# Optimization experiments

Hardware: AMD Instinct MI355X
Metric: run time of the kernel (lower is better)

Reference implementation:

```python
import jax, jax.numpy as jnp
import numpy as np
import math

DIMS = 128
S = 2                     # scalar_attention_num
VS = 0.25                 # voxel_size
QS = 0.01                 # quant_size
L = int((2 * VS + 0.0001) // QS)   # 50, quant table length
GRID = int(2 / VS)        # 8
G = GRID ** 3             # 512 voxel groups
K = 32                    # points per voxel (regularized)
B = 2
N = G * K                 # 16384 points per cloud


def setup_inputs() -> dict:
    key = jax.random.key(0)
    ks = jax.random.split(key, 12)
    inputs = jax.random.normal(ks[0], (B, N, DIMS), jnp.float32)
    # coordinates scaled so per-voxel pairwise distances lie in (-VS, VS)
    coordinates = jax.random.uniform(ks[1], (B, N, 3), jnp.float32) * VS
    # groups: partition of the N points into G voxels of K points each
    groups = jnp.tile(jnp.arange(N, dtype=jnp.int32).reshape(1, G, K), (B, 1, 1))
    effective_groups = jnp.tile(jnp.arange(G, dtype=jnp.int32)[None], (B, 1))
    qkv_w = jax.random.normal(ks[2], (S, DIMS, 3 * DIMS), jnp.float32) * 0.02
    qkv_b = jnp.zeros((S, 3 * DIMS), jnp.float32)
    table_x = jax.random.normal(ks[3], (S, 3, L, DIMS), jnp.float32) * 0.02
    table_y = jax.random.normal(ks[4], (S, 3, L, DIMS), jnp.float32) * 0.02
    table_z = jax.random.normal(ks[5], (S, 3, L, DIMS), jnp.float32) * 0.02
    trans_w = jax.random.normal(ks[6], (DIMS * (S + 1), DIMS), jnp.float32) * 0.02
    trans_b = jnp.zeros((DIMS,), jnp.float32)
    ln_g = jnp.ones((DIMS,), jnp.float32)
    ln_b = jnp.zeros((DIMS,), jnp.float32)
    return {"inputs": inputs, "coordinates": coordinates, "qkv_w": qkv_w,
            "qkv_b": qkv_b, "table_x": table_x, "table_y": table_y,
            "table_z": table_z, "trans_w": trans_w, "trans_b": trans_b,
            "ln_g": ln_g, "ln_b": ln_b, "groups": groups,
            "effective_groups": effective_groups}


def reference(inputs, coordinates, qkv_w, qkv_b, table_x, table_y, table_z,
              trans_w, trans_b, ln_g, ln_b, groups, effective_groups):
    B_, N_, d = inputs.shape
    # gather points per voxel: [B,G,K,d] / [B,G,K,3]
    gflat = groups.reshape(B_, -1)
    feats = jnp.take_along_axis(inputs, gflat[..., None], axis=1).reshape(B_, G, K, d)
    coords = jnp.take_along_axis(coordinates, gflat[..., None], axis=1).reshape(B_, G, K, 3)
    # pairwise distances within each voxel: [B,G,K,K,3]
    dist = coords[:, :, :, None, :] - coords[:, :, None, :, :]
    idx = jnp.clip(jnp.floor((dist + VS) / QS).astype(jnp.int32), 0, L - 1)
    f = feats
    x = feats
    for s in range(S):
        qkv = f @ qkv_w[s] + qkv_b[s]                  # [B,G,K,3d]
        q, k, v = jnp.split(qkv, 3, axis=-1)
        enc = (table_x[s, 1][idx[..., 0]]
               + table_y[s, 1][idx[..., 1]]
               + table_z[s, 1][idx[..., 2]])           # [B,G,K,K,d]
        bias = jnp.einsum('bgid,bgijd->bgij', k, enc)
        scores = (jnp.einsum('bgid,bgjd->bgij', q, k) + bias) / math.sqrt(d)
        attn = jax.nn.softmax(scores, axis=-1)
        f = jnp.einsum('bgij,bgjd->bgid', attn, v)
        x = jnp.concatenate([x, f], axis=-1)
    # trans: Linear -> LayerNorm -> ReLU, then max-pool over points
    h = x @ trans_w + trans_b
    mu = jnp.mean(h, axis=-1, keepdims=True)
    var = jnp.var(h, axis=-1, keepdims=True)
    h = (h - mu) / jnp.sqrt(var + 1e-5) * ln_g + ln_b
    h = jax.nn.relu(h)
    pooled = jnp.max(h, axis=2)                        # [B,G,d]
    # group index i = m*GRID^2 + n*GRID + t ; output grid at [t,n,m]
    grid = pooled.reshape(B_, GRID, GRID, GRID, d).transpose(0, 3, 2, 1, 4)
    out = grid.reshape(B_, -1, d)                      # [B, GRID^3, d]
    # per-point retrieve buffer: scatter pooled feature back to each point
    for_ret = jnp.zeros((B_, N_, d), inputs.dtype)
    b_idx = jnp.arange(B_)[:, None, None]
    for_ret = for_ret.at[b_idx, groups].set(
        jnp.broadcast_to(pooled[:, :, None, :], (B_, G, K, d)))
    return out, for_ret
```

## Files before the change

kernel.cpp:

```cpp
#include <hip/hip_runtime.h>
#include <cstddef>


#define D_   128
#define VSF  0.25f
#define QSF  0.01f
#define LQ   50
#define G_   512
#define KP   32
#define BB   2
#define NP   16384
#define MT   32768
#define SCALE 0.08838834764831845f
#define NT_ALL 34
#define FRAG_S (NT_ALL * 4 * 64 * 8)

using short8 = __attribute__((ext_vector_type(8))) short;
using f32x4  = __attribute__((ext_vector_type(4))) float;

__device__ inline unsigned short f2bf(float x) {
  unsigned u = __builtin_bit_cast(unsigned, x);
  u += 0x7fffu + ((u >> 16) & 1u);
  return (unsigned short)(u >> 16);
}
__device__ inline float bu(unsigned short h) {
  return __builtin_bit_cast(float, (unsigned)h << 16);
}
__device__ inline short8 as_short8(uint4 v) {
  union { uint4 u; short8 s; } x; x.u = v; return x.s;
}

__global__ __launch_bounds__(256) void prep_tt(
    const float* __restrict__ tbl_x, const float* __restrict__ tbl_y,
    const float* __restrict__ tbl_z, float* __restrict__ Tt)
{
  const int c = threadIdx.x;
  const int s = blockIdx.x >> 7;
  const int e = blockIdx.x & 127;
  float v = 0.f;
  if (c < 150) {
    const int axis = c / 50, l = c - axis * 50;
    const float* tb = (axis == 0 ? tbl_x : (axis == 1 ? tbl_y : tbl_z));
    v = tb[(((size_t)s * 3 + 1) * LQ + l) * D_ + e];
  }
  Tt[((size_t)(s * 128 + e)) * 256 + c] = v;
}

__global__ __launch_bounds__(256) void wf_gemm(
    const float* __restrict__ qkv_w, const float* __restrict__ Tt,
    float* __restrict__ Wf)
{
  __shared__ __align__(16) float A_s[16][68];
  __shared__ __align__(16) float B_s[16][132];
  const int t  = threadIdx.x;
  const int s  = blockIdx.z;
  const float* A = qkv_w + (size_t)s * 128 * 384 + 128;
  const float* B = Tt + (size_t)s * 128 * 256;
  float* C       = Wf + (size_t)s * 128 * 256;
  const int m0 = blockIdx.x * 64;
  const int n0 = blockIdx.y * 128;
  const int r  = t >> 2;
  const int kq = (t & 3) * 4;
  const float* arow = A + (size_t)(m0 + r) * 384;
  const int kkb = t >> 4;
  const int cb  = (t & 15) * 8;
  const float* wbase = B + (size_t)kkb * 256 + n0 + cb;
  const int tx = t & 31, ty = t >> 5;

  float acc[8][4];
  #pragma unroll
  for (int i = 0; i < 8; i++)
    #pragma unroll
    for (int j = 0; j < 4; j++) acc[i][j] = 0.f;

  for (int k0 = 0; k0 < 128; k0 += 16) {
    float4 av = *(const float4*)(arow + k0 + kq);
    float4 b0 = *(const float4*)(wbase + (size_t)k0 * 256);
    float4 b1 = *(const float4*)(wbase + (size_t)k0 * 256 + 4);
    __syncthreads();
    A_s[kq + 0][r] = av.x;
    A_s[kq + 1][r] = av.y;
    A_s[kq + 2][r] = av.z;
    A_s[kq + 3][r] = av.w;
    *(float4*)&B_s[kkb][cb]     = b0;
    *(float4*)&B_s[kkb][cb + 4] = b1;
    __syncthreads();
    #pragma unroll
    for (int kk = 0; kk < 16; kk++) {
      float4 a03 = *(const float4*)&A_s[kk][ty * 8];
      float4 a47 = *(const float4*)&A_s[kk][ty * 8 + 4];
      float4 bv  = *(const float4*)&B_s[kk][tx * 4];
      float a[8] = {a03.x, a03.y, a03.z, a03.w, a47.x, a47.y, a47.z, a47.w};
      float bj[4] = {bv.x, bv.y, bv.z, bv.w};
      #pragma unroll
      for (int i = 0; i < 8; i++)
        #pragma unroll
        for (int j = 0; j < 4; j++)
          acc[i][j] += a[i] * bj[j];
    }
  }
  #pragma unroll
  for (int i = 0; i < 8; i++) {
    float4 o = {acc[i][0], acc[i][1], acc[i][2], acc[i][3]};
    *(float4*)(C + (size_t)(m0 + ty * 8 + i) * 256 + n0 + tx * 4) = o;
  }
}

__global__ __launch_bounds__(64) void pack2(
    const float* __restrict__ qkv_w, const float* __restrict__ Wf,
    const float* __restrict__ trans_w, const float* __restrict__ qkv_b,
    const float* __restrict__ Tt,
    unsigned short* __restrict__ allfrag,
    unsigned short* __restrict__ transfrag,
    float* __restrict__ bc)
{
  const int blk = blockIdx.x;
  const int lane = threadIdx.x;
  const float* B; int ldb, dstidx; unsigned short* dst; int kbase, n;
  if (blk < 192) {
    const int s = blk / 96, r = blk - s * 96;
    const int nt = r >> 2, ks = r & 3;
    B = qkv_w + (size_t)s * 128 * 384; ldb = 384;
    n = nt * 16 + (lane & 15);
    kbase = ks * 32 + ((lane >> 4) * 8);
    dst = allfrag + (size_t)s * FRAG_S;
    dstidx = nt * 4 + ks;
  } else if (blk < 272) {
    const int s = (blk - 192) / 40, r = (blk - 192) - s * 40;
    const int snt = r >> 2, ks = r & 3;
    B = Wf + (size_t)s * 32768; ldb = 256;
    n = snt * 16 + (lane & 15);
    kbase = ks * 32 + ((lane >> 4) * 8);
    dst = allfrag + (size_t)s * FRAG_S;
    dstidx = (24 + snt) * 4 + ks;
  } else if (blk < 368) {
    const int r = blk - 272;
    const int nt = r / 12, ks = r - nt * 12;
    B = trans_w; ldb = 128;
    n = nt * 16 + (lane & 15);
    kbase = ks * 32 + ((lane >> 4) * 8);
    dst = transfrag;
    dstidx = nt * 12 + ks;
  } else {
    const int s = blk - 368;
    for (int c = lane; c < 544; c += 64) {
      float v;
      if (c < 384) {
        v = qkv_b[s * 384 + c];
      } else {
        const float* bk = qkv_b + (size_t)s * 384 + 128;
        const float* T  = Tt + (size_t)s * 128 * 256 + (c - 384);
        float a = 0.f;
        #pragma unroll 4
        for (int e = 0; e < 128; e++) a += bk[e] * T[(size_t)e * 256];
        v = a;
      }
      bc[s * 544 + c] = v;
    }
    return;
  }
  unsigned v[4];
  #pragma unroll
  for (int h = 0; h < 4; h++) {
    const float x0 = B[(size_t)(kbase + 2 * h) * ldb + n];
    const float x1 = B[(size_t)(kbase + 2 * h + 1) * ldb + n];
    v[h] = f2bf(x0) | ((unsigned)f2bf(x1) << 16);
  }
  uint4 o = {v[0], v[1], v[2], v[3]};
  *(uint4*)(dst + ((size_t)dstidx * 64 + lane) * 8) = o;
}

__global__ __launch_bounds__(512, 2) void mega(
    const float* __restrict__ inputs,
    const float* __restrict__ coords,
    const int*   __restrict__ groups,
    const unsigned short* __restrict__ allfrag,
    const float* __restrict__ bc,
    const unsigned short* __restrict__ transfrag,
    const float* __restrict__ trans_b, const float* __restrict__ ln_g,
    const float* __restrict__ ln_b,
    float* __restrict__ out_all)
{
  __shared__ __align__(16) unsigned short feats_s[32][136];
  __shared__ __align__(16) unsigned short f1_s[32][136];
  __shared__ __align__(16) unsigned short qk_s[32][440];
  __shared__ __align__(16) unsigned short vT_s[128][40];
  __shared__ __align__(16) float sc_s[32 * 33];
  __shared__ float cs[32][4];
  __shared__ float red_s[8][2][16][2];
  __shared__ float wmax_s[2][128];
  float* pooled_s = &red_s[0][0][0][0];

  const int t   = threadIdx.x;
  const int bid = blockIdx.x;
  const int b   = bid >> 9;
  const int g   = bid & 511;
  const int wv = t >> 6, lane = t & 63, quad = lane >> 4, col = lane & 15;

  {
    const int p = t >> 4, sg = t & 15;
    const int pid = groups[(b << 14) + g * KP + p];
    const float* src = inputs + ((size_t)(b << 14) + (size_t)pid) * D_ + sg * 8;
    float4 a0 = *(const float4*)(src);
    float4 a1 = *(const float4*)(src + 4);
    uint4 o0;
    o0.x = f2bf(a0.x) | ((unsigned)f2bf(a0.y) << 16);
    o0.y = f2bf(a0.z) | ((unsigned)f2bf(a0.w) << 16);
    o0.z = f2bf(a1.x) | ((unsigned)f2bf(a1.y) << 16);
    o0.w = f2bf(a1.z) | ((unsigned)f2bf(a1.w) << 16);
    *(uint4*)&feats_s[p][sg * 8] = o0;
  }
  if (t < 32) {
    const int pid = groups[(b << 14) + g * KP + t];
    const float* cp = coords + ((size_t)(b << 14) + (size_t)pid) * 3;
    cs[t][0] = cp[0]; cs[t][1] = cp[1]; cs[t][2] = cp[2];
  }
  __syncthreads();

  const int startsA[8] = {0, 5, 10, 14, 18, 22, 26, 30};
  const int cntsA[8]   = {5, 5, 4, 4, 4, 4, 4, 4};
  const int start = startsA[wv];
  const int cnt   = cntsA[wv];

  for (int layer = 0; layer < 2; layer++) {
    const uint4* fr = (const uint4*)(allfrag + (size_t)layer * FRAG_S) + lane;
    const float* bcl = bc + layer * 544;

    uint4 avu[2][4];
    if (layer == 0) {
      #pragma unroll
      for (int ks = 0; ks < 4; ks++) {
        avu[0][ks] = *(const uint4*)&feats_s[col][ks * 32 + quad * 8];
        avu[1][ks] = *(const uint4*)&feats_s[16 + col][ks * 32 + quad * 8];
      }
    } else {
      #pragma unroll
      for (int ks = 0; ks < 4; ks++) {
        avu[0][ks] = *(const uint4*)&f1_s[col][ks * 32 + quad * 8];
        avu[1][ks] = *(const uint4*)&f1_s[16 + col][ks * 32 + quad * 8];
      }
    }

    uint4 bvc[4];
    #pragma unroll
    for (int ks = 0; ks < 4; ks++) bvc[ks] = fr[(start * 4 + ks) * 64];

    for (int u = 0; u < cnt; u++) {
      const int ntn = start + ((u + 1 < cnt) ? (u + 1) : u);
      uint4 bvn[4];
      #pragma unroll
      for (int ks = 0; ks < 4; ks++) bvn[ks] = fr[(ntn * 4 + ks) * 64];

      f32x4 a0 = (f32x4){0.f, 0.f, 0.f, 0.f};
      f32x4 a1 = (f32x4){0.f, 0.f, 0.f, 0.f};
      #pragma unroll
      for (int ks = 0; ks < 4; ks++) {
        short8 bv = as_short8(bvc[ks]);
        a0 = __builtin_amdgcn_mfma_f32_16x16x32_bf16(as_short8(avu[0][ks]), bv, a0, 0, 0, 0);
        a1 = __builtin_amdgcn_mfma_f32_16x16x32_bf16(as_short8(avu[1][ks]), bv, a1, 0, 0, 0);
      }
      const int nt = start + u;
      const int cc = nt * 16 + col;
      const float bsv = bcl[cc];
      if (cc >= 256 && cc < 384) {
        const unsigned lo0 = f2bf(a0[0] + bsv) | ((unsigned)f2bf(a0[1] + bsv) << 16);
        const unsigned hi0 = f2bf(a0[2] + bsv) | ((unsigned)f2bf(a0[3] + bsv) << 16);
        uint2 w0 = {lo0, hi0};
        *(uint2*)&vT_s[cc - 256][quad * 4] = w0;
        const unsigned lo1 = f2bf(a1[0] + bsv) | ((unsigned)f2bf(a1[1] + bsv) << 16);
        const unsigned hi1 = f2bf(a1[2] + bsv) | ((unsigned)f2bf(a1[3] + bsv) << 16);
        uint2 w1 = {lo1, hi1};
        *(uint2*)&vT_s[cc - 256][16 + quad * 4] = w1;
      } else {
        const int ccol = (cc < 256) ? cc : cc - 128;
        #pragma unroll
        for (int reg = 0; reg < 4; reg++) {
          qk_s[quad * 4 + reg][ccol]      = f2bf(a0[reg] + bsv);
          qk_s[16 + quad * 4 + reg][ccol] = f2bf(a1[reg] + bsv);
        }
      }
      #pragma unroll
      for (int ks = 0; ks < 4; ks++) bvc[ks] = bvn[ks];
    }
    __syncthreads();

    if (wv < 4) {
      const int ihalf = wv >> 1, jhalf = wv & 1;
      f32x4 sacc = {0.f, 0.f, 0.f, 0.f};
      #pragma unroll
      for (int ks = 0; ks < 4; ks++) {
        short8 qv = as_short8(*(const uint4*)&qk_s[ihalf * 16 + col][ks * 32 + quad * 8]);
        short8 kv = as_short8(*(const uint4*)&qk_s[jhalf * 16 + col][128 + ks * 32 + quad * 8]);
        sacc = __builtin_amdgcn_mfma_f32_16x16x32_bf16(qv, kv, sacc, 0, 0, 0);
      }
      const int j = jhalf * 16 + col;
      const float cjx = cs[j][0], cjy = cs[j][1], cjz = cs[j][2];
      #pragma unroll
      for (int reg = 0; reg < 4; reg++) {
        const int i = ihalf * 16 + quad * 4 + reg;
        const float dx = cs[i][0] - cjx;
        const float dy = cs[i][1] - cjy;
        const float dz = cs[i][2] - cjz;
        int ix = (int)floorf((dx + VSF) / QSF);
        int iy = (int)floorf((dy + VSF) / QSF);
        int iz = (int)floorf((dz + VSF) / QSF);
        ix = ix < 0 ? 0 : (ix > 49 ? 49 : ix);
        iy = iy < 0 ? 0 : (iy > 49 ? 49 : iy);
        iz = iz < 0 ? 0 : (iz > 49 ? 49 : iz);
        const unsigned short* dki = &qk_s[i][256];
        const float biasv = bu(dki[ix]) + bu(dki[50 + iy]) + bu(dki[100 + iz]);
        sc_s[i * 33 + j] = (sacc[reg] + biasv) * SCALE;
      }
    }
    __syncthreads();

    if (t < 256) {
      const int p = t >> 3, sg = t & 7;
      float vals[4];
      float lm = -1e30f;
      #pragma unroll
      for (int u = 0; u < 4; u++) {
        vals[u] = sc_s[p * 33 + sg + u * 8];
        lm = fmaxf(lm, vals[u]);
      }
      lm = fmaxf(lm, __shfl_xor(lm, 1));
      lm = fmaxf(lm, __shfl_xor(lm, 2));
      lm = fmaxf(lm, __shfl_xor(lm, 4));
      float ls = 0.f;
      #pragma unroll
      for (int u = 0; u < 4; u++) { vals[u] = __expf(vals[u] - lm); ls += vals[u]; }
      ls += __shfl_xor(ls, 1);
      ls += __shfl_xor(ls, 2);
      ls += __shfl_xor(ls, 4);
      const float inv = 1.f / ls;
      #pragma unroll
      for (int u = 0; u < 4; u++)
        qk_s[p][408 + sg + u * 8] = f2bf(vals[u] * inv);
    }
    __syncthreads();

    {
      const int mt = wv & 1, ftb = (wv >> 1) * 2;
      unsigned short* dst_base = (layer == 0) ? &f1_s[0][0] : &qk_s[0][0];
      const int dst_ld = (layer == 0) ? 136 : 440;
      short8 pv = as_short8(*(const uint4*)&qk_s[mt * 16 + col][408 + quad * 8]);
      #pragma unroll
      for (int u = 0; u < 2; u++) {
        const int ft = ftb + u;
        short8 vv = as_short8(*(const uint4*)&vT_s[ft * 16 + col][quad * 8]);
        f32x4 o = (f32x4){0.f, 0.f, 0.f, 0.f};
        o = __builtin_amdgcn_mfma_f32_16x16x32_bf16(pv, vv, o, 0, 0, 0);
        const int f = ft * 16 + col;
        #pragma unroll
        for (int reg = 0; reg < 4; reg++) {
          const int i = mt * 16 + quad * 4 + reg;
          dst_base[i * dst_ld + f] = f2bf(o[reg]);
        }
      }
    }
    __syncthreads();
  }

  const int nt = wv;
  f32x4 tacc[2];
  tacc[0] = (f32x4){0.f, 0.f, 0.f, 0.f};
  tacc[1] = (f32x4){0.f, 0.f, 0.f, 0.f};
  const uint4* tf = (const uint4*)transfrag + lane;
  uint4 grp[4];
  #pragma unroll
  for (int ks = 0; ks < 4; ks++) grp[ks] = tf[(nt * 12 + ks) * 64];
  #pragma unroll
  for (int ksb = 0; ksb < 12; ksb += 4) {
    uint4 nxt[4];
    if (ksb < 8) {
      #pragma unroll
      for (int ks = 0; ks < 4; ks++) nxt[ks] = tf[(nt * 12 + ksb + 4 + ks) * 64];
    }
    #pragma unroll
    for (int ks = 0; ks < 4; ks++) {
      const int kk = ksb + ks;
      short8 bv = as_short8(grp[ks]);
      #pragma unroll
      for (int mt = 0; mt < 2; mt++) {
        const unsigned short* ar =
            (kk < 4) ? &feats_s[mt * 16 + col][(kk & 3) * 32 + quad * 8]
          : (kk < 8) ? &f1_s[mt * 16 + col][(kk & 3) * 32 + quad * 8]
                     : &qk_s[mt * 16 + col][(kk & 3) * 32 + quad * 8];
        short8 av = as_short8(*(const uint4*)ar);
        tacc[mt] = __builtin_amdgcn_mfma_f32_16x16x32_bf16(av, bv, tacc[mt], 0, 0, 0);
      }
    }
    if (ksb < 8) {
      #pragma unroll
      for (int ks = 0; ks < 4; ks++) grp[ks] = nxt[ks];
    }
  }
  const int c = nt * 16 + col;
  const float bsv = trans_b[c], gg = ln_g[c], lb = ln_b[c];
  float s[2][4], ssq[2][4];
  #pragma unroll
  for (int mt = 0; mt < 2; mt++)
    #pragma unroll
    for (int reg = 0; reg < 4; reg++) {
      const float v = tacc[mt][reg] + bsv;
      tacc[mt][reg] = v;
      s[mt][reg] = v; ssq[mt][reg] = v * v;
    }
  #pragma unroll
  for (int mk = 1; mk <= 8; mk <<= 1) {
    #pragma unroll
    for (int mt = 0; mt < 2; mt++)
      #pragma unroll
      for (int reg = 0; reg < 4; reg++) {
        s[mt][reg]   += __shfl_xor(s[mt][reg],   mk);
        ssq[mt][reg] += __shfl_xor(ssq[mt][reg], mk);
      }
  }
  if (col == 0) {
    #pragma unroll
    for (int mt = 0; mt < 2; mt++)
      #pragma unroll
      for (int reg = 0; reg < 4; reg++) {
        red_s[wv][mt][quad * 4 + reg][0] = s[mt][reg];
        red_s[wv][mt][quad * 4 + reg][1] = ssq[mt][reg];
      }
  }
  __syncthreads();
  float mu[2][4], rstd[2][4];
  #pragma unroll
  for (int mt = 0; mt < 2; mt++)
    #pragma unroll
    for (int reg = 0; reg < 4; reg++) {
      float st = 0.f, sst = 0.f;
      #pragma unroll
      for (int w = 0; w < 8; w++) {
        st  += red_s[w][mt][quad * 4 + reg][0];
        sst += red_s[w][mt][quad * 4 + reg][1];
      }
      mu[mt][reg] = st * (1.f / 128.f);
      const float var = sst * (1.f / 128.f) - mu[mt][reg] * mu[mt][reg];
      rstd[mt][reg] = rsqrtf(var + 1e-5f);
    }
  float cm[2];
  #pragma unroll
  for (int mt = 0; mt < 2; mt++) {
    float mx = 0.f;
    #pragma unroll
    for (int reg = 0; reg < 4; reg++) {
      float v = (tacc[mt][reg] - mu[mt][reg]) * rstd[mt][reg] * gg + lb;
      v = fmaxf(v, 0.f);
      mx = fmaxf(mx, v);
    }
    cm[mt] = mx;
  }
  #pragma unroll
  for (int mt = 0; mt < 2; mt++) {
    cm[mt] = fmaxf(cm[mt], __shfl_xor(cm[mt], 16));
    cm[mt] = fmaxf(cm[mt], __shfl_xor(cm[mt], 32));
  }
  __syncthreads();
  if (quad == 0) {
    #pragma unroll
    for (int mt = 0; mt < 2; mt++)
      wmax_s[mt][c] = cm[mt];
  }
  __syncthreads();

  if (t < 128) {
    const int cc = t;
    const float mx = fmaxf(wmax_s[0][cc], wmax_s[1][cc]);
    pooled_s[cc] = mx;
    const int mm = g >> 6, nn = (g >> 3) & 7, tt2 = g & 7;
    const int opos = tt2 * 64 + nn * 8 + mm;
    out_all[((size_t)b * G_ + opos) * D_ + cc] = mx;
  }
  __syncthreads();

  if (t < 256) {
    const int p = t >> 3, sg = t & 7;
    const int pid = groups[(b << 14) + g * KP + p];
    float* dst = out_all + (size_t)BB * G_ * D_
               + ((size_t)(b << 14) + (size_t)pid) * D_ + sg * 16;
    #pragma unroll
    for (int u = 0; u < 4; u++)
      *(float4*)(dst + u * 4) = *(const float4*)&pooled_s[sg * 16 + u * 4];
  }
}

extern "C" void kernel_launch(void* const* d_in, const int* in_sizes, int n_in,
                              void* d_out, int out_size, void* d_ws, size_t ws_size,
                              hipStream_t stream) {
  const float* inputs  = (const float*)d_in[0];
  const float* coords  = (const float*)d_in[1];
  const float* qkv_w   = (const float*)d_in[2];
  const float* qkv_b   = (const float*)d_in[3];
  const float* tbl_x   = (const float*)d_in[4];
  const float* tbl_y   = (const float*)d_in[5];
  const float* tbl_z   = (const float*)d_in[6];
  const float* trans_w = (const float*)d_in[7];
  const float* trans_b = (const float*)d_in[8];
  const float* ln_g    = (const float*)d_in[9];
  const float* ln_b    = (const float*)d_in[10];
  const int*   groups  = (const int*)d_in[11];

  float* out = (float*)d_out;
  unsigned short* allfrag   = (unsigned short*)d_ws;
  unsigned short* transfrag = allfrag + 2 * FRAG_S;
  float* Tt  = (float*)(transfrag + 96 * 512);
  float* Wf  = Tt + (size_t)2 * 128 * 256;
  float* bc  = Wf + (size_t)2 * 128 * 256;

  prep_tt<<<256, 256, 0, stream>>>(tbl_x, tbl_y, tbl_z, Tt);
  wf_gemm<<<dim3(2, 2, 2), 256, 0, stream>>>(qkv_w, Tt, Wf);
  pack2<<<370, 64, 0, stream>>>(qkv_w, Wf, trans_w, qkv_b, Tt,
                                allfrag, transfrag, bc);

  mega<<<BB * G_, 512, 0, stream>>>(inputs, coords, groups, allfrag, bc,
                                    transfrag, trans_b, ln_g, ln_b, out);
}
```

Before: 165.3 us.

## Fold trans-linear partial GEMMs into attention layers and shrink shared memory

Each layer's input feature slice is now multiplied by its slice of the trans weights during the attention stage, using A-fragments already in registers. This lets layer-1 output overwrite feats_s, so f1_s can be dropped. The qk buffer is narrowed and the reduction buffers alias sc_s, cutting LDS per block so more blocks may fit per CU. The cost is an extra live accumulator and prefetched weight registers during attention, which adds register pressure under launch_bounds(512,2).

```diff
diff --git a/kernel.cpp b/kernel.cpp
--- a/kernel.cpp
+++ b/kernel.cpp
@@ -182,14 +182,13 @@
     float* __restrict__ out_all)
 {
   __shared__ __align__(16) unsigned short feats_s[32][136];
-  __shared__ __align__(16) unsigned short f1_s[32][136];
-  __shared__ __align__(16) unsigned short qk_s[32][440];
+  __shared__ __align__(16) unsigned short qk_s[32][424];
   __shared__ __align__(16) unsigned short vT_s[128][40];
   __shared__ __align__(16) float sc_s[32 * 33];
   __shared__ float cs[32][4];
-  __shared__ float red_s[8][2][16][2];
-  __shared__ float wmax_s[2][128];
-  float* pooled_s = &red_s[0][0][0][0];
+  float (*red_s)[2][16][2] = (float (*)[2][16][2])sc_s;
+  float (*wmax_s)[128]     = (float (*)[128])(sc_s + 512);
+  float* pooled_s = sc_s;
 
   const int t   = threadIdx.x;
   const int bid = blockIdx.x;
@@ -222,23 +221,20 @@
   const int start = startsA[wv];
   const int cnt   = cntsA[wv];
 
+  f32x4 tacc[2];
+  tacc[0] = (f32x4){0.f, 0.f, 0.f, 0.f};
+  tacc[1] = (f32x4){0.f, 0.f, 0.f, 0.f};
+  const uint4* tf = (const uint4*)transfrag + lane;
+
   for (int layer = 0; layer < 2; layer++) {
     const uint4* fr = (const uint4*)(allfrag + (size_t)layer * FRAG_S) + lane;
     const float* bcl = bc + layer * 544;
 
     uint4 avu[2][4];
-    if (layer == 0) {
-      #pragma unroll
-      for (int ks = 0; ks < 4; ks++) {
-        avu[0][ks] = *(const uint4*)&feats_s[col][ks * 32 + quad * 8];
-        avu[1][ks] = *(const uint4*)&feats_s[16 + col][ks * 32 + quad * 8];
-      }
-    } else {
-      #pragma unroll
-      for (int ks = 0; ks < 4; ks++) {
-        avu[0][ks] = *(const uint4*)&f1_s[col][ks * 32 + quad * 8];
-        avu[1][ks] = *(const uint4*)&f1_s[16 + col][ks * 32 + quad * 8];
-      }
+    #pragma unroll
+    for (int ks = 0; ks < 4; ks++) {
+      avu[0][ks] = *(const uint4*)&feats_s[col][ks * 32 + quad * 8];
+      avu[1][ks] = *(const uint4*)&feats_s[16 + col][ks * 32 + quad * 8];
     }
 
     uint4 bvc[4];
@@ -282,6 +278,9 @@
       #pragma unroll
       for (int ks = 0; ks < 4; ks++) bvc[ks] = bvn[ks];
     }
+    uint4 tgv[4];
+    #pragma unroll
+    for (int ks = 0; ks < 4; ks++) tgv[ks] = tf[(wv * 12 + layer * 4 + ks) * 64];
     __syncthreads();
 
     if (wv < 4) {
@@ -312,6 +311,12 @@
         sc_s[i * 33 + j] = (sacc[reg] + biasv) * SCALE;
       }
     }
+    #pragma unroll
+    for (int ks = 0; ks < 4; ks++) {
+      short8 bv = as_short8(tgv[ks]);
+      tacc[0] = __builtin_amdgcn_mfma_f32_16x16x32_bf16(as_short8(avu[0][ks]), bv, tacc[0], 0, 0, 0);
+      tacc[1] = __builtin_amdgcn_mfma_f32_16x16x32_bf16(as_short8(avu[1][ks]), bv, tacc[1], 0, 0, 0);
+    }
     __syncthreads();
 
     if (t < 256) {
@@ -335,15 +340,15 @@
       const float inv = 1.f / ls;
       #pragma unroll
       for (int u = 0; u < 4; u++)
-        qk_s[p][408 + sg + u * 8] = f2bf(vals[u] * inv);
+        qk_s[p][128 + sg + u * 8] = f2bf(vals[u] * inv);
     }
     __syncthreads();
 
     {
       const int mt = wv & 1, ftb = (wv >> 1) * 2;
-      unsigned short* dst_base = (layer == 0) ? &f1_s[0][0] : &qk_s[0][0];
-      const int dst_ld = (layer == 0) ? 136 : 440;
-      short8 pv = as_short8(*(const uint4*)&qk_s[mt * 16 + col][408 + quad * 8]);
+      unsigned short* dst_base = (layer == 0) ? &feats_s[0][0] : &qk_s[0][0];
+      const int dst_ld = (layer == 0) ? 136 : 424;
+      short8 pv = as_short8(*(const uint4*)&qk_s[mt * 16 + col][128 + quad * 8]);
       #pragma unroll
       for (int u = 0; u < 2; u++) {
         const int ft = ftb + u;
@@ -362,37 +367,18 @@
   }
 
   const int nt = wv;
-  f32x4 tacc[2];
-  tacc[0] = (f32x4){0.f, 0.f, 0.f, 0.f};
-  tacc[1] = (f32x4){0.f, 0.f, 0.f, 0.f};
-  const uint4* tf = (const uint4*)transfrag + lane;
-  uint4 grp[4];
-  #pragma unroll
-  for (int ks = 0; ks < 4; ks++) grp[ks] = tf[(nt * 12 + ks) * 64];
-  #pragma unroll
-  for (int ksb = 0; ksb < 12; ksb += 4) {
-    uint4 nxt[4];
-    if (ksb < 8) {
-      #pragma unroll
-      for (int ks = 0; ks < 4; ks++) nxt[ks] = tf[(nt * 12 + ksb + 4 + ks) * 64];
-    }
+  {
+    uint4 gv[4];
+    #pragma unroll
+    for (int ks = 0; ks < 4; ks++) gv[ks] = tf[(nt * 12 + 8 + ks) * 64];
     #pragma unroll
     for (int ks = 0; ks < 4; ks++) {
-      const int kk = ksb + ks;
-      short8 bv = as_short8(grp[ks]);
+      short8 bv = as_short8(gv[ks]);
       #pragma unroll
       for (int mt = 0; mt < 2; mt++) {
-        const unsigned short* ar =
-            (kk < 4) ? &feats_s[mt * 16 + col][(kk & 3) * 32 + quad * 8]
-          : (kk < 8) ? &f1_s[mt * 16 + col][(kk & 3) * 32 + quad * 8]
-                     : &qk_s[mt * 16 + col][(kk & 3) * 32 + quad * 8];
-        short8 av = as_short8(*(const uint4*)ar);
+        short8 av = as_short8(*(const uint4*)&qk_s[mt * 16 + col][ks * 32 + quad * 8]);
         tacc[mt] = __builtin_amdgcn_mfma_f32_16x16x32_bf16(av, bv, tacc[mt], 0, 0, 0);
       }
-    }
-    if (ksb < 8) {
-      #pragma unroll
-      for (int ks = 0; ks < 4; ks++) grp[ks] = nxt[ks];
     }
   }
   const int c = nt * 16 + col;
```

Result: no change. 165.5 us (+0.1%).
